# Kernel optimization log

Measured on AMD Instinct MI355X. Metric: run time of the kernel, lower is better.

The kernel has to match this reference:

```python
import jax, jax.numpy as jnp
import numpy as np

BG_W = 1.0
DILATED_BG_W = 5.0
EDGE_W = 20.0
KSIZE = 3


def setup_inputs() -> dict:
    key = jax.random.key(0)
    k1, k2 = jax.random.split(key)
    B, C, H, W = 16, 1, 1024, 1024
    pred = jax.random.normal(k1, (B, C, H, W), dtype=jnp.float32)
    target = (jax.random.uniform(k2, (B, C, H, W)) < 0.05).astype(jnp.float32)
    return {"pred": pred, "target": target}


def _dilate(target):
    # cv2.dilate with KSIZExKSIZE rect kernel == max pool, stride 1, SAME padding
    return jax.lax.reduce_window(
        target, -jnp.inf, jax.lax.max,
        window_dimensions=(1, 1, KSIZE, KSIZE),
        window_strides=(1, 1, 1, 1),
        padding="SAME",
    )


def reference(pred, target):
    dilated = _dilate(target)
    # weight: edge pixels (target>0.5) -> EDGE_W, else dilated band -> DILATED_BG_W, else BG_W
    weight = jnp.where(target > 0.5, EDGE_W,
                       jnp.where(dilated > 0.5, DILATED_BG_W, BG_W))
    # binary_cross_entropy_with_logits, reduction='none', then mean
    x = pred
    losses = weight * (jnp.maximum(x, 0.0) - x * target + jnp.log1p(jnp.exp(-jnp.abs(x))))
    return jnp.mean(losses)
```

## Files before the change

### kernel.cpp

```cpp
#include <hip/hip_runtime.h>

#define HH 1024
#define WW 1024
#define BAND 8
#define NT 256

__device__ __forceinline__ float fmax3(float a, float b, float c) {
    return fmaxf(a, fmaxf(b, c));
}

__device__ __forceinline__ float loss_elem(float x, float t, float dil) {
    float w = fmaf(15.0f, t, fmaf(4.0f, dil, 1.0f));
    float a  = fabsf(x);
    float sp = __logf(1.0f + __expf(-a));
    return w * (fmaxf(x, 0.0f) - x * t + sp);
}

template <bool PER_WAVE>
__global__ __launch_bounds__(NT, 4) void dilatedweightBCE_main(
        const float* __restrict__ pred,
        const float* __restrict__ target,
        float* __restrict__ partial) {
    __shared__ float swave[NT / 64];

    const int t    = threadIdx.x;
    const int lane = t & 63;
    const int wv   = t >> 6;
    const int c    = t * 4;

    const int l    = blockIdx.x;
    const int xcd  = l & 7;
    const int j    = l >> 3;
    const int img  = j >> 4;
    const int band = j & 15;
    const int h0   = (xcd * 16 + band) * BAND;

    const float* timg = target + (size_t)img * HH * WW;
    const float* pimg = pred   + (size_t)img * HH * WW;
    const float4 zero = make_float4(0.0f, 0.0f, 0.0f, 0.0f);

    float4 tr[BAND + 2];
    tr[0] = (h0 > 0) ? *(const float4*)(timg + (size_t)(h0 - 1) * WW + c) : zero;
    #pragma unroll
    for (int r = 0; r < BAND; ++r)
        tr[r + 1] = *(const float4*)(timg + (size_t)(h0 + r) * WW + c);
    tr[BAND + 1] = (h0 + BAND < HH)
                 ? *(const float4*)(timg + (size_t)(h0 + BAND) * WW + c) : zero;

    float4 xr[BAND];
    #pragma unroll
    for (int r = 0; r < BAND; ++r)
        xr[r] = *(const float4*)(pimg + (size_t)(h0 + r) * WW + c);

    float halo[BAND];
    #pragma unroll
    for (int r = 0; r < BAND; ++r) halo[r] = 0.0f;
    if (lane == 0 || lane == 63) {
        const int pc = (lane == 0) ? c - 1 : c + 4;
        if (pc >= 0 && pc < WW) {
            float hv[BAND + 2];
            hv[0] = (h0 > 0) ? timg[(size_t)(h0 - 1) * WW + pc] : 0.0f;
            #pragma unroll
            for (int r = 0; r < BAND; ++r)
                hv[r + 1] = timg[(size_t)(h0 + r) * WW + pc];
            hv[BAND + 1] = (h0 + BAND < HH)
                         ? timg[(size_t)(h0 + BAND) * WW + pc] : 0.0f;
            #pragma unroll
            for (int r = 0; r < BAND; ++r)
                halo[r] = fmax3(hv[r], hv[r + 1], hv[r + 2]);
        }
    }

    float s = 0.0f;
    #pragma unroll
    for (int r = 0; r < BAND; ++r) {
        float4 a = tr[r], m = tr[r + 1], d = tr[r + 2];
        float4 vm = make_float4(fmax3(a.x, m.x, d.x), fmax3(a.y, m.y, d.y),
                                fmax3(a.z, m.z, d.z), fmax3(a.w, m.w, d.w));

        float lft = __shfl_up(vm.w, 1);
        float rgt = __shfl_down(vm.x, 1);
        if (lane == 0)  lft = halo[r];
        if (lane == 63) rgt = halo[r];

        float d0 = fmax3(lft,  vm.x, vm.y);
        float d1 = fmax3(vm.x, vm.y, vm.z);
        float d2 = fmax3(vm.y, vm.z, vm.w);
        float d3 = fmax3(vm.z, vm.w, rgt);

        float4 x = xr[r];
        s += loss_elem(x.x, m.x, d0);
        s += loss_elem(x.y, m.y, d1);
        s += loss_elem(x.z, m.z, d2);
        s += loss_elem(x.w, m.w, d3);
    }

    #pragma unroll
    for (int off = 32; off > 0; off >>= 1)
        s += __shfl_down(s, off);

    if (PER_WAVE) {
        if (lane == 0)
            partial[(size_t)l * (NT / 64) + wv] = s;
    } else {
        if (lane == 0) swave[wv] = s;
        __syncthreads();
        if (t == 0) {
            float tot = 0.0f;
            #pragma unroll
            for (int i = 0; i < NT / 64; ++i) tot += swave[i];
            partial[l] = tot;
        }
    }
}

__global__ __launch_bounds__(1024) void dilatedweightBCE_reduce(
        const float* __restrict__ partial,
        float* __restrict__ out,
        int npart4,
        float inv_n) {
    __shared__ float swave[16];
    const int t = threadIdx.x;

    float s = 0.0f;
    const float4* p4 = (const float4*)partial;
    for (int i = t; i < npart4; i += 1024) {
        float4 v = p4[i];
        s += v.x + v.y + v.z + v.w;
    }

    #pragma unroll
    for (int off = 32; off > 0; off >>= 1)
        s += __shfl_down(s, off);

    const int lane = t & 63;
    if (lane == 0) swave[t >> 6] = s;
    __syncthreads();
    if (t == 0) {
        float tot = 0.0f;
        #pragma unroll
        for (int i = 0; i < 16; ++i) tot += swave[i];
        out[0] = tot * inv_n;
    }
}

extern "C" void kernel_launch(void* const* d_in, const int* in_sizes, int n_in,
                              void* d_out, int out_size, void* d_ws, size_t ws_size,
                              hipStream_t stream) {
    const float* pred   = (const float*)d_in[0];
    const float* target = (const float*)d_in[1];
    float* out     = (float*)d_out;
    float* partial = (float*)d_ws;

    const int n  = in_sizes[0];
    const int Bn = n / (HH * WW);
    const int nblocks = (HH / BAND) * Bn;

    const size_t need = (size_t)nblocks * (NT / 64) * sizeof(float);
    if (ws_size >= need) {
        dilatedweightBCE_main<true><<<nblocks, NT, 0, stream>>>(pred, target, partial);
        dilatedweightBCE_reduce<<<1, 1024, 0, stream>>>(partial, out,
                                                        nblocks * (NT / 64) / 4,
                                                        1.0f / (float)n);
    } else {
        dilatedweightBCE_main<false><<<nblocks, NT, 0, stream>>>(pred, target, partial);
        dilatedweightBCE_reduce<<<1, 1024, 0, stream>>>(partial, out,
                                                        nblocks / 4,
                                                        1.0f / (float)n);
    }
}
```

Measured before the change: 145.1 us.

## Stream rows through rolling register window with larger slabs per block

```diff
diff --git a/kernel.cpp b/kernel.cpp
--- a/kernel.cpp
+++ b/kernel.cpp
@@ -2,7 +2,7 @@
 
 #define HH 1024
 #define WW 1024
-#define BAND 8
+#define RPB 16
 #define NT 256
 
 __device__ __forceinline__ float fmax3(float a, float b, float c) {
@@ -31,64 +31,74 @@
     const int l    = blockIdx.x;
     const int xcd  = l & 7;
     const int j    = l >> 3;
-    const int img  = j >> 4;
-    const int band = j & 15;
-    const int h0   = (xcd * 16 + band) * BAND;
+    const int img  = j >> 3;
+    const int slab = j & 7;
+    const int h0   = xcd * (8 * RPB) + slab * RPB;
 
     const float* timg = target + (size_t)img * HH * WW;
     const float* pimg = pred   + (size_t)img * HH * WW;
+    const float* tp   = timg + (size_t)h0 * WW + c;
+    const float* pp   = pimg + (size_t)h0 * WW + c;
+
+    const bool top = (h0 > 0);
+    const bool bot = (h0 + RPB < HH);
     const float4 zero = make_float4(0.0f, 0.0f, 0.0f, 0.0f);
 
-    float4 tr[BAND + 2];
-    tr[0] = (h0 > 0) ? *(const float4*)(timg + (size_t)(h0 - 1) * WW + c) : zero;
+    const bool hval = (lane == 0) ? (c > 0) : ((lane == 63) ? (c + 4 < WW) : false);
+    const float* thp = timg + (size_t)h0 * WW + ((lane == 0) ? (c - 1) : (c + 4));
+
+    float4 T[5];
+    float4 X[3];
+    float  hv[5];
     #pragma unroll
-    for (int r = 0; r < BAND; ++r)
-        tr[r + 1] = *(const float4*)(timg + (size_t)(h0 + r) * WW + c);
-    tr[BAND + 1] = (h0 + BAND < HH)
-                 ? *(const float4*)(timg + (size_t)(h0 + BAND) * WW + c) : zero;
+    for (int i = 0; i < 5; ++i) hv[i] = 0.0f;
 
-    float4 xr[BAND];
-    #pragma unroll
-    for (int r = 0; r < BAND; ++r)
-        xr[r] = *(const float4*)(pimg + (size_t)(h0 + r) * WW + c);
-
-    float halo[BAND];
-    #pragma unroll
-    for (int r = 0; r < BAND; ++r) halo[r] = 0.0f;
-    if (lane == 0 || lane == 63) {
-        const int pc = (lane == 0) ? c - 1 : c + 4;
-        if (pc >= 0 && pc < WW) {
-            float hv[BAND + 2];
-            hv[0] = (h0 > 0) ? timg[(size_t)(h0 - 1) * WW + pc] : 0.0f;
-            #pragma unroll
-            for (int r = 0; r < BAND; ++r)
-                hv[r + 1] = timg[(size_t)(h0 + r) * WW + pc];
-            hv[BAND + 1] = (h0 + BAND < HH)
-                         ? timg[(size_t)(h0 + BAND) * WW + pc] : 0.0f;
-            #pragma unroll
-            for (int r = 0; r < BAND; ++r)
-                halo[r] = fmax3(hv[r], hv[r + 1], hv[r + 2]);
-        }
+    T[0] = top ? *(const float4*)(tp - WW) : zero;
+    T[1] = *(const float4*)(tp);
+    T[2] = *(const float4*)(tp + WW);
+    T[3] = *(const float4*)(tp + 2 * WW);
+    X[0] = *(const float4*)(pp);
+    X[1] = *(const float4*)(pp + WW);
+    if (hval) {
+        if (top) hv[0] = *(thp - WW);
+        hv[1] = thp[0];
+        hv[2] = thp[WW];
+        hv[3] = thp[2 * WW];
     }
 
     float s = 0.0f;
     #pragma unroll
-    for (int r = 0; r < BAND; ++r) {
-        float4 a = tr[r], m = tr[r + 1], d = tr[r + 2];
+    for (int r = 0; r < RPB; ++r) {
+        if (r + 3 < RPB) {
+            T[(r + 4) % 5] = *(const float4*)(tp + (size_t)(r + 3) * WW);
+            float hnew = 0.0f;
+            if (hval) hnew = thp[(size_t)(r + 3) * WW];
+            hv[(r + 4) % 5] = hnew;
+        } else if (r + 3 == RPB) {
+            T[(r + 4) % 5] = bot ? *(const float4*)(tp + (size_t)RPB * WW) : zero;
+            float hnew = 0.0f;
+            if (hval && bot) hnew = thp[(size_t)RPB * WW];
+            hv[(r + 4) % 5] = hnew;
+        }
+        if (r + 2 < RPB)
+            X[(r + 2) % 3] = *(const float4*)(pp + (size_t)(r + 2) * WW);
+
+        float4 a = T[r % 5], m = T[(r + 1) % 5], d = T[(r + 2) % 5];
         float4 vm = make_float4(fmax3(a.x, m.x, d.x), fmax3(a.y, m.y, d.y),
                                 fmax3(a.z, m.z, d.z), fmax3(a.w, m.w, d.w));
 
+        float hmax = fmax3(hv[r % 5], hv[(r + 1) % 5], hv[(r + 2) % 5]);
         float lft = __shfl_up(vm.w, 1);
         float rgt = __shfl_down(vm.x, 1);
-        if (lane == 0)  lft = halo[r];
-        if (lane == 63) rgt = halo[r];
+        if (lane == 0)  lft = hmax;
+        if (lane == 63) rgt = hmax;
 
         float d0 = fmax3(lft,  vm.x, vm.y);
         float d1 = fmax3(vm.x, vm.y, vm.z);
         float d2 = fmax3(vm.y, vm.z, vm.w);
         float d3 = fmax3(vm.z, vm.w, rgt);
 
-        float4 x = xr[r];
+        float4 x = X[r % 3];
         s += loss_elem(x.x, m.x, d0);
         s += loss_elem(x.y, m.y, d1);
         s += loss_elem(x.z, m.z, d2);
@@ -154,7 +164,7 @@
 
     const int n  = in_sizes[0];
     const int Bn = n / (HH * WW);
-    const int nblocks = (HH / BAND) * Bn;
+    const int nblocks = (HH / RPB) * Bn;
 
     const size_t need = (size_t)nblocks * (NT / 64) * sizeof(float);
     if (ws_size >= need) {
```

Result: slower. 188.3 us (+29.8%).
